# Kernel optimization log

Hardware: AMD Instinct MI355X
Metric: run time of the kernel (lower is better)

## Reference

```python
import jax, jax.numpy as jnp
import numpy as np

B, L, D_MODEL, HEADS = 4, 2048, 1024, 16
D_K = D_MODEL // HEADS
EPS = 1e-8
ROPE_BASE = 10000.0


def setup_inputs() -> dict:
    key = jax.random.key(0)
    k1, k2, k3 = jax.random.split(key, 3)
    x = jax.random.normal(k1, (B, L, D_MODEL), jnp.float32)
    W_in = jax.random.normal(k2, (3 * D_MODEL, D_MODEL), jnp.float32) * 0.02
    W_o = jax.random.normal(k3, (D_MODEL, D_MODEL), jnp.float32) * 0.02
    return {"x": x, "W_in": W_in, "W_o": W_o}


def _layer_norm(x, eps=EPS):
    # F.layer_norm with no affine params
    mu = jnp.mean(x, axis=-1, keepdims=True)
    var = jnp.var(x, axis=-1, keepdims=True)
    return (x - mu) * jax.lax.rsqrt(var + eps)


def _rope(x):
    # x: [B, H, L, d_k]; interleaved-pair rotary embedding
    seq = x.shape[2]
    half = x.shape[-1] // 2
    inv_freq = 1.0 / (ROPE_BASE ** (jnp.arange(half, dtype=jnp.float32) * 2.0 / x.shape[-1]))
    ang = jnp.arange(seq, dtype=jnp.float32)[:, None] * inv_freq[None, :]  # [L, half]
    cos, sin = jnp.cos(ang), jnp.sin(ang)
    x1, x2 = x[..., 0::2], x[..., 1::2]
    r1 = x1 * cos - x2 * sin
    r2 = x1 * sin + x2 * cos
    return jnp.stack([r1, r2], axis=-1).reshape(x.shape)


def reference(x, W_in, W_o):
    h = _layer_norm(x)
    qkv = h @ W_in.T  # [B, L, 3*D]
    q, k, v = jnp.split(qkv, 3, axis=-1)
    to_heads = lambda t: t.reshape(B, L, HEADS, D_K).transpose(0, 2, 1, 3)  # [B,H,L,dk]
    q, k, v = to_heads(q), to_heads(k), to_heads(v)
    q, k = _rope(q), _rope(k)
    scale = 1.0 / np.sqrt(D_K).astype(np.float32)
    scores = jnp.einsum('bhqd,bhkd->bhqk', q, k) * scale
    causal = jnp.tril(jnp.ones((L, L), dtype=bool))
    scores = jnp.where(causal, scores, -jnp.inf)
    attn = jax.nn.softmax(scores, axis=-1)
    o = jnp.einsum('bhqk,bhkd->bhqd', attn, v)
    o = o.transpose(0, 2, 1, 3).reshape(B, L, D_MODEL)
    return o @ W_o.T
```

## Files before the change

### kernel.cpp

```cpp
#include <hip/hip_runtime.h>
#include <cstdint>

typedef unsigned short u16;
typedef short bf16x8 __attribute__((ext_vector_type(8)));
typedef float f32x4 __attribute__((ext_vector_type(4)));
typedef float f32x16 __attribute__((ext_vector_type(16)));
typedef unsigned int u32x2 __attribute__((ext_vector_type(2)));
typedef unsigned int u32x4 __attribute__((ext_vector_type(4)));

#define NB 4
#define SEQ 2048
#define DMODEL 1024
#define NHEADS 16
#define DHEAD 64
#define BHTOT (NB*NHEADS)
#define MROWS (NB*SEQ)

__device__ __forceinline__ float bf2f(u16 u){
  union { unsigned int i; float f; } x; x.i = ((unsigned int)u)<<16; return x.f;
}
__device__ __forceinline__ u16 f2bf(float f){
  union { float f; unsigned int i; } x; x.f = f;
  unsigned int r = x.i + 0x7fffu + ((x.i>>16)&1u);
  return (u16)(r>>16);
}

typedef const __attribute__((address_space(1))) unsigned int* gas_t;
typedef __attribute__((address_space(3))) unsigned int* las_t;
__device__ __forceinline__ void async_cp16(const void* g, void* l){
  __builtin_amdgcn_global_load_lds((gas_t)g, (las_t)l, 16, 0, 0);
}

__device__ __forceinline__ void plswap(unsigned int &a, unsigned int &b){
#if __has_builtin(__builtin_amdgcn_permlane32_swap)
  u32x2 r = __builtin_amdgcn_permlane32_swap(a, b, false, false);
  a = r[0]; b = r[1];
#else
  asm("v_permlane32_swap_b32 %0, %1" : "+v"(a), "+v"(b));
#endif
}

__global__ __launch_bounds__(256) void cast2_kernel(const float* __restrict__ wa, u16* __restrict__ oa,
    const float* __restrict__ wb, u16* __restrict__ ob, int na4){
  int i = blockIdx.x*256 + threadIdx.x;
  const float* src; u16* dst; int j;
  if(i < na4){ src = wa; dst = oa; j = i; }
  else       { src = wb; dst = ob; j = i - na4; }
  float4 v = ((const float4*)src)[j];
  ushort4 o;
  o.x=f2bf(v.x); o.y=f2bf(v.y); o.z=f2bf(v.z); o.w=f2bf(v.w);
  ((ushort4*)dst)[j] = o;
}

__global__ __launch_bounds__(256) void ln_kernel(const float* __restrict__ x, u16* __restrict__ h){
  int row = blockIdx.x;
  const float* xr = x + (size_t)row*DMODEL;
  u16* hr = h + (size_t)row*DMODEL;
  int t = threadIdx.x;
  float4 v = ((const float4*)xr)[t];
  float f0=v.x, f1=v.y, f2=v.z, f3=v.w;
  float s = f0+f1+f2+f3;
  float q = f0*f0+f1*f1+f2*f2+f3*f3;
  #pragma unroll
  for(int off=32; off; off>>=1){ s += __shfl_xor(s, off); q += __shfl_xor(q, off); }
  __shared__ float ss[4], sq[4];
  int wv = t>>6, lane = t&63;
  if(lane==0){ ss[wv]=s; sq[wv]=q; }
  __syncthreads();
  s = ss[0]+ss[1]+ss[2]+ss[3];
  q = sq[0]+sq[1]+sq[2]+sq[3];
  float mu  = s * (1.0f/DMODEL);
  float var = q * (1.0f/DMODEL) - mu*mu;
  float rs  = rsqrtf(var + 1e-8f);
  ushort4 o;
  o.x=f2bf((f0-mu)*rs); o.y=f2bf((f1-mu)*rs); o.z=f2bf((f2-mu)*rs); o.w=f2bf((f3-mu)*rs);
  ((ushort4*)hr)[t] = o;
}

#define BM 128
#define BN 128
#define BK 32

template<int MODE>
__global__ __launch_bounds__(256) void gemm_bt(const u16* __restrict__ A, const u16* __restrict__ Bm,
    u16* __restrict__ Qb, u16* __restrict__ Kb, u16* __restrict__ Vtb, float* __restrict__ outf,
    int M, int N, int K){
  __shared__ u16 As[BM*BK];
  __shared__ u16 Bs[BN*BK];
  int t = threadIdx.x;
  int lane = t&63, wv = t>>6;
  int c = lane&15, g = lane>>4;
  int wm = wv>>1, wn = wv&1;
  int m0 = blockIdx.y*BM, n0 = blockIdx.x*BN;
  f32x4 acc[4][4] = {};
  for(int k0=0;k0<K;k0+=BK){
    __syncthreads();
    #pragma unroll
    for(int i=0;i<2;i++){
      int e = t*8 + i*2048;
      int r = e>>5, col = e&31;
      async_cp16(&A [(size_t)(m0+r)*K + k0 + col], &As[e]);
      async_cp16(&Bm[(size_t)(n0+r)*K + k0 + col], &Bs[e]);
    }
    __syncthreads();
    bf16x8 af[4], bfr[4];
    #pragma unroll
    for(int i=0;i<4;i++){
      af[i]  = *(const bf16x8*)(&As[(wm*64 + i*16 + c)*BK + g*8]);
      bfr[i] = *(const bf16x8*)(&Bs[(wn*64 + i*16 + c)*BK + g*8]);
    }
    #pragma unroll
    for(int mi=0;mi<4;mi++)
      #pragma unroll
      for(int ni=0;ni<4;ni++)
        acc[mi][ni] = __builtin_amdgcn_mfma_f32_16x16x32_bf16(af[mi], bfr[ni], acc[mi][ni], 0,0,0);
  }
  if(MODE==1){
    #pragma unroll
    for(int mi=0;mi<4;mi++){
      int mrow = m0 + wm*64 + mi*16 + g*4;
      #pragma unroll
      for(int ni=0;ni<4;ni++){
        int ncol = n0 + wn*64 + ni*16 + c;
        #pragma unroll
        for(int r=0;r<4;r++)
          outf[(size_t)(mrow+r)*N + ncol] = acc[mi][ni][r];
      }
    }
  } else {
    #pragma unroll
    for(int ni=0;ni<4;ni++){
      int n = n0 + wn*64 + ni*16 + c;
      int sel = n>>10, head = (n>>6)&15, d = n&63;
      #pragma unroll
      for(int mi=0;mi<4;mi++){
        int m = m0 + wm*64 + mi*16 + g*4;
        int b = m>>11, l = m&(SEQ-1);
        if(sel<2){
          u16* dst = (sel==0?Qb:Kb) + ((size_t)((b*NHEADS+head)*SEQ + l))*DHEAD + d;
          #pragma unroll
          for(int r=0;r<4;r++) dst[(size_t)r*DHEAD] = f2bf(acc[mi][ni][r]);
        } else {
          ushort4 pk;
          pk.x=f2bf(acc[mi][ni][0]); pk.y=f2bf(acc[mi][ni][1]);
          pk.z=f2bf(acc[mi][ni][2]); pk.w=f2bf(acc[mi][ni][3]);
          *(ushort4*)(&Vtb[((size_t)((b*NHEADS+head)*DHEAD + d))*SEQ + l]) = pk;
        }
      }
    }
  }
}

#define SC2 0.180336879f
__global__ __launch_bounds__(256) void rope_kernel(u16* __restrict__ Q, u16* __restrict__ Kb){
  int tid = blockIdx.x*256 + threadIdx.x;
  int j = tid&31, l = tid>>5;
  float inv = exp2f(-(float)j * (13.28771237954945f/32.0f));
  float sn, cs;
  sincosf((float)l*inv, &sn, &cs);
  size_t base = (size_t)l*DHEAD + 2*j;
  #pragma unroll 4
  for(int bh=0; bh<BHTOT; bh++){
    size_t off = base + (size_t)bh*SEQ*DHEAD;
    ushort2 q2 = *(ushort2*)(&Q[off]);
    float x1=bf2f(q2.x), x2=bf2f(q2.y);
    ushort2 o;
    o.x = f2bf((x1*cs - x2*sn)*SC2); o.y = f2bf((x1*sn + x2*cs)*SC2);
    *(ushort2*)(&Q[off]) = o;
    ushort2 k2 = *(ushort2*)(&Kb[off]);
    x1=bf2f(k2.x); x2=bf2f(k2.y);
    o.x = f2bf(x1*cs - x2*sn); o.y = f2bf(x1*sn + x2*cs);
    *(ushort2*)(&Kb[off]) = o;
  }
}


#define QKS32(KF) { \
  f32x16 z_ = {}; \
  z_ = __builtin_amdgcn_mfma_f32_32x32x16_bf16(KF[0], qf[0], z_, 0,0,0); \
  z_ = __builtin_amdgcn_mfma_f32_32x32x16_bf16(KF[1], qf[1], z_, 0,0,0); \
  z_ = __builtin_amdgcn_mfma_f32_32x32x16_bf16(KF[2], qf[2], z_, 0,0,0); \
  z_ = __builtin_amdgcn_mfma_f32_32x32x16_bf16(KF[3], qf[3], z_, 0,0,0); \
  sc = z_; }

#define LDK { \
  _Pragma("unroll") for(int dk_=0;dk_<4;dk_++){ \
    int kb_ = (c32*128 + dk_*32 + hl*16) ^ ((c32&7)<<4); \
    kf[dk_] = *(const bf16x8*)((const char*)(&Kls[cur][0]) + kb_); } }

#define LDV { \
  _Pragma("unroll") for(int dt_=0;dt_<2;dt_++) \
    _Pragma("unroll") for(int ks_=0;ks_<2;ks_++){ \
      int d_ = dt_*32 + c32; \
      int vb_ = (d_*64 + ks_*32 + hl*16) ^ (((d_>>1)&7)<<4); \
      vf[dt_][ks_] = *(const bf16x8*)((const char*)(&Vls[cur][0]) + vb_); } }

#define EXPPACK(MASKED) { \
  unsigned int pk_[8]; \
  _Pragma("unroll") for(int j_=0;j_<8;j_++){ \
    float a_ = exp2f(sc[2*j_]); \
    float b_ = exp2f(sc[2*j_+1]); \
    if(MASKED){ \
      int k0_ = ((2*j_)&3)   + 8*((2*j_)>>2)   + 4*hl; \
      int k1_ = ((2*j_+1)&3) + 8*((2*j_+1)>>2) + 4*hl; \
      a_ = (k0_ <= c32) ? a_ : 0.f; \
      b_ = (k1_ <= c32) ? b_ : 0.f; } \
    lrow += a_ + b_; \
    asm("v_cvt_pk_bf16_f32 %0, %1, %2" : "=v"(pk_[j_]) : "v"(a_), "v"(b_)); } \
  plswap(pk_[0], pk_[2]); \
  plswap(pk_[1], pk_[3]); \
  plswap(pk_[4], pk_[6]); \
  plswap(pk_[5], pk_[7]); \
  u32x4 wa_ = { pk_[0], pk_[1], pk_[2], pk_[3] }; \
  u32x4 wb_ = { pk_[4], pk_[5], pk_[6], pk_[7] }; \
  pa0 = __builtin_bit_cast(bf16x8, wa_); \
  pa1 = __builtin_bit_cast(bf16x8, wb_); }

#define PVM32 { \
  oacc0 = __builtin_amdgcn_mfma_f32_32x32x16_bf16(pa0, vf[0][0], oacc0, 0,0,0); \
  oacc0 = __builtin_amdgcn_mfma_f32_32x32x16_bf16(pa1, vf[0][1], oacc0, 0,0,0); \
  oacc1 = __builtin_amdgcn_mfma_f32_32x32x16_bf16(pa0, vf[1][0], oacc1, 0,0,0); \
  oacc1 = __builtin_amdgcn_mfma_f32_32x32x16_bf16(pa1, vf[1][1], oacc1, 0,0,0); }

__global__ __launch_bounds__(512, 4) void attn_kernel(const u16* __restrict__ Q, const u16* __restrict__ Kb,
    const u16* __restrict__ Vt, u16* __restrict__ O){
  __shared__ u16 Kls[2][2048];
  __shared__ u16 Vls[2][2048];
  __shared__ float Ls[8][32];
  int t = threadIdx.x, lane = t&63, w = t>>6;
  int c32 = lane&31, hl = lane>>5, h8 = hl*8;
  int bh = blockIdx.x;
  int b = bh>>4, hh = bh&15;
  int g = 7 - blockIdx.y;
  int s = g*8 + w;
  int wrow = s*32;
  int NT = g*8 + 8;
  const u16* Qp = Q  + (size_t)bh*SEQ*DHEAD;
  const u16* Kp = Kb + (size_t)bh*SEQ*DHEAD;
  const u16* Vp = Vt + (size_t)bh*DHEAD*SEQ;

  bool isK = (w < 4);
  int cch = isK ? t : (t - 256);
  int prow = cch>>3;
  int jsrc = (cch&7) ^ (prow&7);
  size_t soff0, sstep;
  if(isK){
    soff0 = (size_t)prow*64 + (size_t)jsrc*8;
    sstep = 32*64;
  } else {
    int c2 = prow*8 + jsrc;
    soff0 = (size_t)(c2>>2)*SEQ + (size_t)(c2&3)*8;
    sstep = 32;
  }
  const u16* sbase = isK ? Kp : Vp;

  bf16x8 qf[4];
  #pragma unroll
  for(int dk=0;dk<4;dk++)
    qf[dk] = *(const bf16x8*)(&Qp[(size_t)(wrow + c32)*DHEAD + dk*16 + h8]);

  f32x16 oacc0 = {}, oacc1 = {};
  float lrow = 0.f;
  f32x16 sc;
  bf16x8 kf[4], vf[2][2], pa0, pa1;

  {
    u16* dst = isK ? &Kls[0][cch*8] : &Vls[0][cch*8];
    async_cp16(sbase + soff0, dst);
  }
  int cur = 0;
  #pragma unroll 1
  for(int tt=0; tt<NT; ++tt){
    __syncthreads();
    if(tt+1 < NT){
      u16* dst = isK ? &Kls[cur^1][cch*8] : &Vls[cur^1][cch*8];
      async_cp16(sbase + soff0 + (size_t)(tt+1)*sstep, dst);
    }
    if(tt <= s){
      LDK; LDV;
      QKS32(kf);
      if(tt == s){ EXPPACK(1); } else { EXPPACK(0); }
      PVM32;
    }
    cur ^= 1;
  }

  float lr = lrow + __shfl_xor(lrow, 32);
  __syncthreads();
  if(hl==0) Ls[w][c32] = lr;
  __syncthreads();
  #pragma unroll
  for(int r=0;r<16;r++){
    int row = (r&3)+8*(r>>2)+4*hl;
    float linv = 1.0f/Ls[w][row];
    size_t o = ((size_t)(b*SEQ + wrow + row))*DMODEL + hh*DHEAD;
    O[o + c32]      = f2bf(oacc0[r]*linv);
    O[o + 32 + c32] = f2bf(oacc1[r]*linv);
  }
}

extern "C" void kernel_launch(void* const* d_in, const int* in_sizes, int n_in,
                              void* d_out, int out_size, void* d_ws, size_t ws_size,
                              hipStream_t stream){
  const float* x    = (const float*)d_in[0];
  const float* W_in = (const float*)d_in[1];
  const float* W_o  = (const float*)d_in[2];
  u16* ws = (u16*)d_ws;
  const size_t T16 = (size_t)8*1024*1024;
  u16* h   = ws;
  u16* Qb  = ws +   T16;
  u16* Kb  = ws + 2*T16;
  u16* Vtb = ws + 3*T16;
  u16* Wb  = ws + 4*T16;
  u16* Wob = Wb + (size_t)3*DMODEL*DMODEL;
  u16* Ob  = h;
  float* out = (float*)d_out;

  const int na4 = 3*DMODEL*DMODEL/4;
  const int nb4 = DMODEL*DMODEL/4;
  cast2_kernel<<<dim3((na4+nb4)/256), dim3(256), 0, stream>>>(W_in, Wb, W_o, Wob, na4);
  ln_kernel<<<dim3(MROWS), dim3(256), 0, stream>>>(x, h);
  gemm_bt<0><<<dim3(3*DMODEL/BN, MROWS/BM), dim3(256), 0, stream>>>(
      h, Wb, Qb, Kb, Vtb, nullptr, MROWS, 3*DMODEL, DMODEL);
  rope_kernel<<<dim3(SEQ*32/256), dim3(256), 0, stream>>>(Qb, Kb);
  attn_kernel<<<dim3(BHTOT, 8), dim3(512), 0, stream>>>(Qb, Kb, Vtb, Ob);
  gemm_bt<1><<<dim3(DMODEL/BN, MROWS/BM), dim3(256), 0, stream>>>(
      Ob, Wob, nullptr, nullptr, nullptr, out, MROWS, DMODEL, DMODEL);
}
```

Measured before the change: 287.9 us.

## Double-buffer GEMM shared-memory tiles with XOR-swizzled layout

The bf16 GEMM kernel now keeps two shared-memory buffers for A and B. It prefetches the next K-slice with async copies while the MFMAs run on the current one, which drops one barrier per iteration. The tile layout in shared memory is XOR-swizzled so the fragment reads avoid bank conflicts. The cost is double the LDS use per block, which may lower occupancy, and more complex index arithmetic.

```diff
diff --git a/kernel.cpp b/kernel.cpp
--- a/kernel.cpp
+++ b/kernel.cpp
@@ -85,35 +85,54 @@
 __global__ __launch_bounds__(256) void gemm_bt(const u16* __restrict__ A, const u16* __restrict__ Bm,
     u16* __restrict__ Qb, u16* __restrict__ Kb, u16* __restrict__ Vtb, float* __restrict__ outf,
     int M, int N, int K){
-  __shared__ u16 As[BM*BK];
-  __shared__ u16 Bs[BN*BK];
+  __shared__ u16 As[2][BM*BK];
+  __shared__ u16 Bs[2][BN*BK];
   int t = threadIdx.x;
   int lane = t&63, wv = t>>6;
   int c = lane&15, g = lane>>4;
   int wm = wv>>1, wn = wv&1;
   int m0 = blockIdx.y*BM, n0 = blockIdx.x*BN;
+
+  int p0 = t>>3,        j0 = t&7;        int js0 = j0 ^ (p0&7);
+  int p1 = (t+256)>>3,  j1 = t&7;        int js1 = j1 ^ (p1&7);
+  size_t aoff0 = (size_t)(p0*2 + (js0>>2))*K + (js0&3)*8;
+  size_t aoff1 = (size_t)(p1*2 + (js1>>2))*K + (js1&3)*8;
+  const u16* Abase = A  + (size_t)m0*K;
+  const u16* Bbase = Bm + (size_t)n0*K;
+
   f32x4 acc[4][4] = {};
+
+  async_cp16(Abase + aoff0, &As[0][t*8]);
+  async_cp16(Abase + aoff1, &As[0][(t+256)*8]);
+  async_cp16(Bbase + aoff0, &Bs[0][t*8]);
+  async_cp16(Bbase + aoff1, &Bs[0][(t+256)*8]);
+
+  int cur = 0;
   for(int k0=0;k0<K;k0+=BK){
     __syncthreads();
-    #pragma unroll
-    for(int i=0;i<2;i++){
-      int e = t*8 + i*2048;
-      int r = e>>5, col = e&31;
-      async_cp16(&A [(size_t)(m0+r)*K + k0 + col], &As[e]);
-      async_cp16(&Bm[(size_t)(n0+r)*K + k0 + col], &Bs[e]);
-    }
-    __syncthreads();
+    if(k0+BK < K){
+      int nb = cur^1;
+      async_cp16(Abase + (k0+BK) + aoff0, &As[nb][t*8]);
+      async_cp16(Abase + (k0+BK) + aoff1, &As[nb][(t+256)*8]);
+      async_cp16(Bbase + (k0+BK) + aoff0, &Bs[nb][t*8]);
+      async_cp16(Bbase + (k0+BK) + aoff1, &Bs[nb][(t+256)*8]);
+    }
     bf16x8 af[4], bfr[4];
     #pragma unroll
     for(int i=0;i<4;i++){
-      af[i]  = *(const bf16x8*)(&As[(wm*64 + i*16 + c)*BK + g*8]);
-      bfr[i] = *(const bf16x8*)(&Bs[(wn*64 + i*16 + c)*BK + g*8]);
+      int ra = wm*64 + i*16 + c;
+      int qa = ((ra&1)*4 + g) ^ ((ra>>1)&7);
+      af[i]  = *(const bf16x8*)(&As[cur][(ra>>1)*64 + qa*8]);
+      int rb = wn*64 + i*16 + c;
+      int qb = ((rb&1)*4 + g) ^ ((rb>>1)&7);
+      bfr[i] = *(const bf16x8*)(&Bs[cur][(rb>>1)*64 + qb*8]);
     }
     #pragma unroll
     for(int mi=0;mi<4;mi++)
       #pragma unroll
       for(int ni=0;ni<4;ni++)
         acc[mi][ni] = __builtin_amdgcn_mfma_f32_16x16x32_bf16(af[mi], bfr[ni], acc[mi][ni], 0,0,0);
+    cur ^= 1;
   }
   if(MODE==1){
     #pragma unroll
```

New measurement: 274.3 us. -4.7%, faster.
